# Performance work log

Hardware: AMD Instinct MI355X
Metric: run time of the kernel (lower is better)

## Reference

```python
import jax, jax.numpy as jnp
import numpy as np

N = 50000      # nodes
E = 600000     # edges
B = 64         # graphs in batch
DIN = 128      # input_dim
DH = 128       # hidden_dim
P = 32         # perm_length
C = 2          # num_classes
K = 2          # TAGConv hops (DGL default)


def setup_inputs() -> dict:
    key = jax.random.key(0)
    ks = jax.random.split(key, 12)
    h = jax.random.normal(ks[0], (N, DIN), dtype=jnp.float32)
    src = jax.random.randint(ks[1], (E,), 0, N, dtype=jnp.int64)
    dst = jax.random.randint(ks[2], (E,), 0, N, dtype=jnp.int64)
    graph_ids = jnp.sort(jax.random.randint(ks[3], (N,), 0, B, dtype=jnp.int64))
    perm_features = jax.random.normal(ks[4], (B, P), dtype=jnp.float32)
    s1 = 1.0 / np.sqrt((K + 1) * DIN)
    s2 = 1.0 / np.sqrt((K + 1) * DH)
    sc = 1.0 / np.sqrt(DH + P)
    W1 = jax.random.uniform(ks[5], ((K + 1) * DIN, DH), jnp.float32, -s1, s1)
    b1 = jax.random.uniform(ks[6], (DH,), jnp.float32, -s1, s1)
    W2 = jax.random.uniform(ks[7], ((K + 1) * DH, DH), jnp.float32, -s2, s2)
    b2 = jax.random.uniform(ks[8], (DH,), jnp.float32, -s2, s2)
    Wc = jax.random.uniform(ks[9], (DH + P, C), jnp.float32, -sc, sc)
    bc = jax.random.uniform(ks[10], (C,), jnp.float32, -sc, sc)
    return {"h": h, "src": src, "dst": dst, "graph_ids": graph_ids,
            "perm_features": perm_features, "W1": W1, "b1": b1,
            "W2": W2, "b2": b2, "Wc": Wc, "bc": bc}


def _tag_conv(x, src, dst, norm, W, b):
    feats = [x]
    for _ in range(K):
        m = jax.ops.segment_sum((feats[-1] * norm)[src], dst, num_segments=N)
        feats.append(m * norm)
    return jnp.concatenate(feats, axis=-1) @ W + b


def reference(h, src, dst, graph_ids, perm_features, W1, b1, W2, b2, Wc, bc):
    # symmetric norm from in-degrees, clamped at 1 (DGL convention)
    deg = jax.ops.segment_sum(jnp.ones((E,), h.dtype), dst, num_segments=N)
    norm = jnp.where(deg < 1.0, 1.0, deg)[:, None] ** -0.5  # [N,1]
    x = jax.nn.relu(_tag_conv(h, src, dst, norm, W1, b1))
    x = _tag_conv(x, src, dst, norm, W2, b2)
    # mean_nodes over batched graph
    sums = jax.ops.segment_sum(x, graph_ids, num_segments=B)          # [B,DH]
    cnt = jax.ops.segment_sum(jnp.ones((N,), x.dtype), graph_ids, num_segments=B)
    hg = sums / jnp.maximum(cnt, 1.0)[:, None]
    combined = jnp.concatenate([hg, perm_features], axis=1)           # [B,DH+P]
    return combined @ Wc + bc
```

## Files before the change

### kernel.cpp

```cpp
#include <hip/hip_runtime.h>

#define N_NODES 50000
#define N_EDGES 600000
#define B_GRAPHS 64
#define DH 128
#define PFEAT 32
#define NCLS 2
#define SCAN_BLOCKS ((N_NODES + 255) / 256)
#define NPAD (N_NODES + 128)

typedef __attribute__((ext_vector_type(8))) short short8v;
typedef __attribute__((ext_vector_type(4))) float float4v;
typedef __attribute__((ext_vector_type(4))) unsigned int uint4v;

__device__ __forceinline__ unsigned int f2bf(float f) {
    unsigned int u = __float_as_uint(f);
    return (u + 0x7FFFu + ((u >> 16) & 1u)) >> 16;
}
__device__ __forceinline__ float bflo(unsigned int p) { return __uint_as_float(p << 16); }
__device__ __forceinline__ float bfhi(unsigned int p) { return __uint_as_float(p & 0xFFFF0000u); }

__global__ void k_cvt(const float* __restrict__ in, unsigned short* __restrict__ outb, int n4) {
    int t = blockIdx.x * blockDim.x + threadIdx.x;
    if (t < n4) {
        float4 v = ((const float4*)in)[t];
        unsigned int lo = f2bf(v.x) | (f2bf(v.y) << 16);
        unsigned int hi = f2bf(v.z) | (f2bf(v.w) << 16);
        uint2 r; r.x = lo; r.y = hi;
        ((uint2*)outb)[t] = r;
    }
}

__global__ void k_cvt_w(const float* __restrict__ W, unsigned short* __restrict__ Wt) {
    int t = blockIdx.x * blockDim.x + threadIdx.x;
    if (t < 384 * 128) {
        int k = t >> 7, c = t & 127;
        Wt[c * 384 + k] = (unsigned short)f2bf(W[t]);
    }
}

__global__ void k_deg(const int* __restrict__ dst, int* __restrict__ deg) {
    int e = blockIdx.x * blockDim.x + threadIdx.x;
    if (e < N_EDGES) atomicAdd(&deg[dst[e]], 1);
}

__global__ void k_norm(const int* __restrict__ deg, float* __restrict__ norm) {
    int n = blockIdx.x * blockDim.x + threadIdx.x;
    if (n < N_NODES) {
        int d = deg[n];
        if (d < 1) d = 1;
        norm[n] = rsqrtf((float)d);
    }
}

__global__ void k_bound(const int* __restrict__ gid, int* __restrict__ gstart) {
    int n = blockIdx.x * blockDim.x + threadIdx.x;
    if (n < N_NODES) {
        int g = gid[n];
        if (n == 0 || gid[n - 1] != g) gstart[g] = n;
    }
}

__global__ void k_bsum(const int* __restrict__ deg, int* __restrict__ bsum) {
    __shared__ int s[256];
    int i = blockIdx.x * 256 + threadIdx.x;
    s[threadIdx.x] = (i < N_NODES) ? deg[i] : 0;
    __syncthreads();
    for (int off = 128; off > 0; off >>= 1) {
        if (threadIdx.x < off) s[threadIdx.x] += s[threadIdx.x + off];
        __syncthreads();
    }
    if (threadIdx.x == 0) bsum[blockIdx.x] = s[0];
}

__global__ void k_bscan(int* __restrict__ bsum) {
    __shared__ int s[256];
    int v = (threadIdx.x < SCAN_BLOCKS) ? bsum[threadIdx.x] : 0;
    s[threadIdx.x] = v;
    __syncthreads();
    for (int off = 1; off < 256; off <<= 1) {
        int t = (threadIdx.x >= off) ? s[threadIdx.x - off] : 0;
        __syncthreads();
        s[threadIdx.x] += t;
        __syncthreads();
    }
    if (threadIdx.x < SCAN_BLOCKS) bsum[threadIdx.x] = s[threadIdx.x] - v;
}

__global__ void k_scan2(const int* __restrict__ deg, const int* __restrict__ bsum,
                        int* __restrict__ row_ptr) {
    __shared__ int s[256];
    int i = blockIdx.x * 256 + threadIdx.x;
    int v = (i < N_NODES) ? deg[i] : 0;
    s[threadIdx.x] = v;
    __syncthreads();
    for (int off = 1; off < 256; off <<= 1) {
        int t = (threadIdx.x >= off) ? s[threadIdx.x - off] : 0;
        __syncthreads();
        s[threadIdx.x] += t;
        __syncthreads();
    }
    if (i < N_NODES) row_ptr[i + 1] = s[threadIdx.x] + bsum[blockIdx.x];
    if (i == 0) row_ptr[0] = 0;
}

__global__ void k_scatter(const int* __restrict__ src, const int* __restrict__ dst,
                          const int* __restrict__ row_ptr, int* __restrict__ cnt,
                          int* __restrict__ col) {
    int e = blockIdx.x * blockDim.x + threadIdx.x;
    if (e < N_EDGES) {
        int d = dst[e];
        int pos = atomicAdd(&cnt[d], 1);
        col[row_ptr[d] + pos] = src[e];
    }
}

__global__ __launch_bounds__(256) void k_spmm(const unsigned short* __restrict__ fin,
                                              const float* __restrict__ norm,
                                              const int* __restrict__ row_ptr,
                                              const int* __restrict__ col,
                                              unsigned short* __restrict__ fout) {
    int wave = threadIdx.x >> 6;
    int lane = threadIdx.x & 63;
    int grp = lane >> 4;
    int l15 = lane & 15;
    int v = blockIdx.x * 4 + wave;
    if (v >= N_NODES) return;
    int beg = row_ptr[v], end = row_ptr[v + 1];

    float a0[8], a1[8];
#pragma unroll
    for (int j = 0; j < 8; ++j) { a0[j] = 0.f; a1[j] = 0.f; }

    for (int base = beg; base < end; base += 8) {
        int e0 = base + grp;
        int e1 = base + 4 + grp;
        int ec0 = (e0 < end) ? e0 : end - 1;
        int ec1 = (e1 < end) ? e1 : end - 1;
        int u0 = col[ec0];
        int u1 = col[ec1];
        uint4v r0 = *(const uint4v*)(fin + (size_t)u0 * 128 + l15 * 8);
        uint4v r1 = *(const uint4v*)(fin + (size_t)u1 * 128 + l15 * 8);
        float w0 = (e0 < end) ? norm[u0] : 0.f;
        float w1 = (e1 < end) ? norm[u1] : 0.f;
#pragma unroll
        for (int q = 0; q < 4; ++q) {
            a0[2 * q]     = fmaf(bflo(r0[q]), w0, a0[2 * q]);
            a0[2 * q + 1] = fmaf(bfhi(r0[q]), w0, a0[2 * q + 1]);
            a1[2 * q]     = fmaf(bflo(r1[q]), w1, a1[2 * q]);
            a1[2 * q + 1] = fmaf(bfhi(r1[q]), w1, a1[2 * q + 1]);
        }
    }

#pragma unroll
    for (int j = 0; j < 8; ++j) {
        float s = a0[j] + a1[j];
        s += __shfl_xor(s, 16, 64);
        s += __shfl_xor(s, 32, 64);
        a0[j] = s;
    }
    if (grp == 0) {
        float nv = norm[v];
        uint4v o;
#pragma unroll
        for (int q = 0; q < 4; ++q)
            o[q] = f2bf(a0[2 * q] * nv) | (f2bf(a0[2 * q + 1] * nv) << 16);
        *(uint4v*)(fout + (size_t)v * 128 + l15 * 8) = o;
    }
}

template <bool RELU, bool POOL>
__global__ __launch_bounds__(256) void k_gemm_mfma(const unsigned short* __restrict__ A0,
                                                   const unsigned short* __restrict__ A1,
                                                   const unsigned short* __restrict__ A2,
                                                   const unsigned short* __restrict__ Wt,
                                                   const float* __restrict__ bias,
                                                   unsigned short* __restrict__ out,
                                                   const int* __restrict__ gid,
                                                   float* __restrict__ gsum) {
    __shared__ float red4[4][128];
    int tid = threadIdx.x;
    int lane = tid & 63;
    int wid = tid >> 6;
    int l15 = lane & 15;
    int lk = lane >> 4;
    int n0 = blockIdx.x * 128;
    int rbase = n0 + wid * 32;

    float4v acc[2][8];
#pragma unroll
    for (int rt = 0; rt < 2; ++rt)
#pragma unroll
        for (int ct = 0; ct < 8; ++ct)
#pragma unroll
            for (int i = 0; i < 4; ++i) acc[rt][ct][i] = 0.f;

    const unsigned short* Aseg[3] = {A0, A1, A2};
#pragma unroll
    for (int ks = 0; ks < 12; ++ks) {
        const unsigned short* A = Aseg[ks >> 2];
        int kloc = (ks & 3) * 32 + lk * 8;
        short8v a0 = *(const short8v*)(A + (size_t)(rbase + l15) * 128 + kloc);
        short8v a1 = *(const short8v*)(A + (size_t)(rbase + 16 + l15) * 128 + kloc);
        const unsigned short* wp = Wt + (size_t)l15 * 384 + ks * 32 + lk * 8;
#pragma unroll
        for (int ct = 0; ct < 8; ++ct) {
            short8v b = *(const short8v*)(wp + (size_t)ct * 16 * 384);
            acc[0][ct] = __builtin_amdgcn_mfma_f32_16x16x32_bf16(a0, b, acc[0][ct], 0, 0, 0);
            acc[1][ct] = __builtin_amdgcn_mfma_f32_16x16x32_bf16(a1, b, acc[1][ct], 0, 0, 0);
        }
    }

    if (!POOL) {
        float bj[8];
#pragma unroll
        for (int ct = 0; ct < 8; ++ct) bj[ct] = bias[ct * 16 + l15];
#pragma unroll
        for (int rt = 0; rt < 2; ++rt)
#pragma unroll
            for (int i = 0; i < 4; ++i) {
                int row = rbase + rt * 16 + lk * 4 + i;
                if (row < N_NODES) {
#pragma unroll
                    for (int ct = 0; ct < 8; ++ct) {
                        float v = acc[rt][ct][i] + bj[ct];
                        if (RELU) v = fmaxf(v, 0.f);
                        out[(size_t)row * 128 + ct * 16 + l15] = (unsigned short)f2bf(v);
                    }
                }
            }
    } else {
        int gr[2][4];
#pragma unroll
        for (int rt = 0; rt < 2; ++rt)
#pragma unroll
            for (int i = 0; i < 4; ++i) {
                int row = rbase + rt * 16 + lk * 4 + i;
                gr[rt][i] = (row < N_NODES) ? gid[row] : -1;
            }
        int lastrow = n0 + 127;
        if (lastrow >= N_NODES) lastrow = N_NODES - 1;
        int gfirst = gid[n0];
        int glast = gid[lastrow];
        for (int g = gfirst; g <= glast; ++g) {
            float p[8];
#pragma unroll
            for (int ct = 0; ct < 8; ++ct) {
                float s = 0.f;
#pragma unroll
                for (int rt = 0; rt < 2; ++rt)
#pragma unroll
                    for (int i = 0; i < 4; ++i)
                        if (gr[rt][i] == g) s += acc[rt][ct][i];
                p[ct] = s;
            }
#pragma unroll
            for (int ct = 0; ct < 8; ++ct) {
                p[ct] += __shfl_xor(p[ct], 16, 64);
                p[ct] += __shfl_xor(p[ct], 32, 64);
            }
            if (lane < 16) {
#pragma unroll
                for (int ct = 0; ct < 8; ++ct) red4[wid][ct * 16 + lane] = p[ct];
            }
            __syncthreads();
            if (tid < 128) {
                float s = red4[0][tid] + red4[1][tid] + red4[2][tid] + red4[3][tid];
                atomicAdd(&gsum[g * 128 + tid], s);
            }
            __syncthreads();
        }
    }
}

__global__ void k_final(const float* __restrict__ gsum, const int* __restrict__ gstart,
                        const float* __restrict__ b2, const float* __restrict__ perm,
                        const float* __restrict__ Wc, const float* __restrict__ bc,
                        float* __restrict__ out) {
    int t = threadIdx.x;
    if (t >= B_GRAPHS * NCLS) return;
    int b = t / NCLS, c = t % NCLS;
    int s = gstart[b];
    float cf = 1.f;
    bool nonempty = (s >= 0);
    if (nonempty) {
        int nxt = N_NODES;
        for (int j = b + 1; j < B_GRAPHS; ++j) {
            int sj = gstart[j];
            if (sj >= 0) { nxt = sj; break; }
        }
        int cnt = nxt - s;
        cf = (cnt < 1) ? 1.f : (float)cnt;
    }
    float acc = bc[c];
    for (int d = 0; d < DH; ++d) {
        float hg = gsum[b * 128 + d] / cf + (nonempty ? b2[d] : 0.f);
        acc += hg * Wc[d * NCLS + c];
    }
    for (int p = 0; p < PFEAT; ++p) acc += perm[b * PFEAT + p] * Wc[(DH + p) * NCLS + c];
    out[t] = acc;
}

extern "C" void kernel_launch(void* const* d_in, const int* in_sizes, int n_in,
                              void* d_out, int out_size, void* d_ws, size_t ws_size,
                              hipStream_t stream) {
    const float* h    = (const float*)d_in[0];
    const int*   src  = (const int*)d_in[1];
    const int*   dst  = (const int*)d_in[2];
    const int*   gid  = (const int*)d_in[3];
    const float* perm = (const float*)d_in[4];
    const float* W1   = (const float*)d_in[5];
    const float* b1   = (const float*)d_in[6];
    const float* W2   = (const float*)d_in[7];
    const float* b2   = (const float*)d_in[8];
    const float* Wc   = (const float*)d_in[9];
    const float* bc   = (const float*)d_in[10];
    float* out = (float*)d_out;

    char* ws = (char*)d_ws;
    size_t off = 0;
    auto alloc = [&](size_t bytes) {
        void* p = ws + off;
        off = (off + bytes + 255) & ~(size_t)255;
        return p;
    };
    int*   deg     = (int*)alloc(N_NODES * 4);
    int*   cnt     = (int*)alloc(N_NODES * 4);
    int*   row_ptr = (int*)alloc((N_NODES + 1) * 4);
    int*   col     = (int*)alloc(N_EDGES * 4);
    int*   bsum    = (int*)alloc(SCAN_BLOCKS * 4);
    float* norm    = (float*)alloc(N_NODES * 4);
    unsigned short* h_bf = (unsigned short*)alloc((size_t)NPAD * 128 * 2);
    unsigned short* f1   = (unsigned short*)alloc((size_t)NPAD * 128 * 2);
    unsigned short* f2   = (unsigned short*)alloc((size_t)NPAD * 128 * 2);
    unsigned short* x2   = (unsigned short*)alloc((size_t)NPAD * 128 * 2);
    unsigned short* Wt1  = (unsigned short*)alloc(384 * 128 * 2);
    unsigned short* Wt2  = (unsigned short*)alloc(384 * 128 * 2);
    float* gsum    = (float*)alloc(B_GRAPHS * 128 * 4);
    int*   gstart  = (int*)alloc(B_GRAPHS * 4);

    hipMemsetAsync(deg, 0, N_NODES * 4, stream);
    hipMemsetAsync(cnt, 0, N_NODES * 4, stream);
    hipMemsetAsync(gsum, 0, B_GRAPHS * 128 * 4, stream);
    hipMemsetAsync(gstart, 0xFF, B_GRAPHS * 4, stream);

    k_cvt<<<(N_NODES * 128 / 4 + 255) / 256, 256, 0, stream>>>(h, h_bf, N_NODES * 128 / 4);
    k_cvt_w<<<(384 * 128 + 255) / 256, 256, 0, stream>>>(W1, Wt1);
    k_cvt_w<<<(384 * 128 + 255) / 256, 256, 0, stream>>>(W2, Wt2);

    k_deg<<<(N_EDGES + 255) / 256, 256, 0, stream>>>(dst, deg);
    k_norm<<<(N_NODES + 255) / 256, 256, 0, stream>>>(deg, norm);
    k_bound<<<(N_NODES + 255) / 256, 256, 0, stream>>>(gid, gstart);
    k_bsum<<<SCAN_BLOCKS, 256, 0, stream>>>(deg, bsum);
    k_bscan<<<1, 256, 0, stream>>>(bsum);
    k_scan2<<<SCAN_BLOCKS, 256, 0, stream>>>(deg, bsum, row_ptr);
    k_scatter<<<(N_EDGES + 255) / 256, 256, 0, stream>>>(src, dst, row_ptr, cnt, col);

    int spmm_grid = (N_NODES + 3) / 4;
    int gemm_grid = (N_NODES + 127) / 128;

    k_spmm<<<spmm_grid, 256, 0, stream>>>(h_bf, norm, row_ptr, col, f1);
    k_spmm<<<spmm_grid, 256, 0, stream>>>(f1, norm, row_ptr, col, f2);
    k_gemm_mfma<true, false><<<gemm_grid, 256, 0, stream>>>(h_bf, f1, f2, Wt1, b1, x2, gid, gsum);

    k_spmm<<<spmm_grid, 256, 0, stream>>>(x2, norm, row_ptr, col, f1);
    k_spmm<<<spmm_grid, 256, 0, stream>>>(f1, norm, row_ptr, col, f2);
    k_gemm_mfma<false, true><<<gemm_grid, 256, 0, stream>>>(x2, f1, f2, Wt2, nullptr, nullptr, gid, gsum);

    k_final<<<1, 128, 0, stream>>>(gsum, gstart, b2, perm, Wc, bc, out);
}
```

Before: 278.5 us.

## Fuse preprocessing kernels and memsets; unroll SpMM edge loop to four accumulators

Merges the four memsets, the input and weight bf16 conversions, the degree count and graph-boundary detection, and the norm computation with the block sum into three kernels, cutting about eight launches from the preprocessing chain. The SpMM inner loop now handles 16 edges per iteration with four independent accumulator sets, so more gather loads are in flight per wave. The cost is more registers in the SpMM kernel and more wasted clamped loads for low-degree nodes, since the average degree is about 12.

```diff
diff --git a/kernel.cpp b/kernel.cpp
--- a/kernel.cpp
+++ b/kernel.cpp
@@ -8,6 +8,8 @@
 #define NCLS 2
 #define SCAN_BLOCKS ((N_NODES + 255) / 256)
 #define NPAD (N_NODES + 128)
+#define NCVT4 (N_NODES * 128 / 4)
+#define WELEMS (384 * 128)
 
 typedef __attribute__((ext_vector_type(8))) short short8v;
 typedef __attribute__((ext_vector_type(4))) float float4v;
@@ -20,51 +22,50 @@
 __device__ __forceinline__ float bflo(unsigned int p) { return __uint_as_float(p << 16); }
 __device__ __forceinline__ float bfhi(unsigned int p) { return __uint_as_float(p & 0xFFFF0000u); }
 
-__global__ void k_cvt(const float* __restrict__ in, unsigned short* __restrict__ outb, int n4) {
-    int t = blockIdx.x * blockDim.x + threadIdx.x;
-    if (t < n4) {
-        float4 v = ((const float4*)in)[t];
+__global__ void k_init(const float* __restrict__ h, unsigned short* __restrict__ h_bf,
+                       const float* __restrict__ W1, const float* __restrict__ W2,
+                       unsigned short* __restrict__ Wt1, unsigned short* __restrict__ Wt2,
+                       int* __restrict__ deg, int* __restrict__ cnt,
+                       float* __restrict__ gsum, int* __restrict__ gstart) {
+    int t = blockIdx.x * 256 + threadIdx.x;
+    if (t < NCVT4) {
+        float4 v = ((const float4*)h)[t];
         unsigned int lo = f2bf(v.x) | (f2bf(v.y) << 16);
         unsigned int hi = f2bf(v.z) | (f2bf(v.w) << 16);
         uint2 r; r.x = lo; r.y = hi;
-        ((uint2*)outb)[t] = r;
-    }
-}
-
-__global__ void k_cvt_w(const float* __restrict__ W, unsigned short* __restrict__ Wt) {
-    int t = blockIdx.x * blockDim.x + threadIdx.x;
-    if (t < 384 * 128) {
-        int k = t >> 7, c = t & 127;
-        Wt[c * 384 + k] = (unsigned short)f2bf(W[t]);
-    }
-}
-
-__global__ void k_deg(const int* __restrict__ dst, int* __restrict__ deg) {
-    int e = blockIdx.x * blockDim.x + threadIdx.x;
-    if (e < N_EDGES) atomicAdd(&deg[dst[e]], 1);
-}
-
-__global__ void k_norm(const int* __restrict__ deg, float* __restrict__ norm) {
-    int n = blockIdx.x * blockDim.x + threadIdx.x;
-    if (n < N_NODES) {
-        int d = deg[n];
-        if (d < 1) d = 1;
-        norm[n] = rsqrtf((float)d);
-    }
-}
-
-__global__ void k_bound(const int* __restrict__ gid, int* __restrict__ gstart) {
-    int n = blockIdx.x * blockDim.x + threadIdx.x;
-    if (n < N_NODES) {
+        ((uint2*)h_bf)[t] = r;
+    }
+    if (t < 2 * WELEMS) {
+        bool second = (t >= WELEMS);
+        int idx = second ? t - WELEMS : t;
+        const float* W = second ? W2 : W1;
+        unsigned short* Wt = second ? Wt2 : Wt1;
+        int k = idx >> 7, c = idx & 127;
+        Wt[c * 384 + k] = (unsigned short)f2bf(W[idx]);
+    }
+    if (t < N_NODES) { deg[t] = 0; cnt[t] = 0; }
+    if (t < B_GRAPHS * DH) gsum[t] = 0.f;
+    if (t < B_GRAPHS) gstart[t] = -1;
+}
+
+__global__ void k_deg_bound(const int* __restrict__ dst, const int* __restrict__ gid,
+                            int* __restrict__ deg, int* __restrict__ gstart) {
+    int t = blockIdx.x * 256 + threadIdx.x;
+    if (t < N_EDGES) atomicAdd(&deg[dst[t]], 1);
+    int n = t - N_EDGES;
+    if (n >= 0 && n < N_NODES) {
         int g = gid[n];
         if (n == 0 || gid[n - 1] != g) gstart[g] = n;
     }
 }
 
-__global__ void k_bsum(const int* __restrict__ deg, int* __restrict__ bsum) {
+__global__ void k_norm_bsum(const int* __restrict__ deg, float* __restrict__ norm,
+                            int* __restrict__ bsum) {
     __shared__ int s[256];
     int i = blockIdx.x * 256 + threadIdx.x;
-    s[threadIdx.x] = (i < N_NODES) ? deg[i] : 0;
+    int d = (i < N_NODES) ? deg[i] : 0;
+    if (i < N_NODES) norm[i] = rsqrtf((float)(d < 1 ? 1 : d));
+    s[threadIdx.x] = d;
     __syncthreads();
     for (int off = 128; off > 0; off >>= 1) {
         if (threadIdx.x < off) s[threadIdx.x] += s[threadIdx.x + off];
@@ -128,33 +129,43 @@
     if (v >= N_NODES) return;
     int beg = row_ptr[v], end = row_ptr[v + 1];
 
-    float a0[8], a1[8];
-#pragma unroll
-    for (int j = 0; j < 8; ++j) { a0[j] = 0.f; a1[j] = 0.f; }
-
-    for (int base = beg; base < end; base += 8) {
+    float a0[8], a1[8], a2[8], a3[8];
+#pragma unroll
+    for (int j = 0; j < 8; ++j) { a0[j] = 0.f; a1[j] = 0.f; a2[j] = 0.f; a3[j] = 0.f; }
+
+    for (int base = beg; base < end; base += 16) {
         int e0 = base + grp;
-        int e1 = base + 4 + grp;
-        int ec0 = (e0 < end) ? e0 : end - 1;
-        int ec1 = (e1 < end) ? e1 : end - 1;
-        int u0 = col[ec0];
-        int u1 = col[ec1];
+        int e1 = e0 + 4, e2 = e0 + 8, e3 = e0 + 12;
+        int last = end - 1;
+        int c0 = (e0 < end) ? e0 : last;
+        int c1 = (e1 < end) ? e1 : last;
+        int c2 = (e2 < end) ? e2 : last;
+        int c3 = (e3 < end) ? e3 : last;
+        int u0 = col[c0], u1 = col[c1], u2 = col[c2], u3 = col[c3];
         uint4v r0 = *(const uint4v*)(fin + (size_t)u0 * 128 + l15 * 8);
         uint4v r1 = *(const uint4v*)(fin + (size_t)u1 * 128 + l15 * 8);
+        uint4v r2 = *(const uint4v*)(fin + (size_t)u2 * 128 + l15 * 8);
+        uint4v r3 = *(const uint4v*)(fin + (size_t)u3 * 128 + l15 * 8);
         float w0 = (e0 < end) ? norm[u0] : 0.f;
         float w1 = (e1 < end) ? norm[u1] : 0.f;
+        float w2 = (e2 < end) ? norm[u2] : 0.f;
+        float w3 = (e3 < end) ? norm[u3] : 0.f;
 #pragma unroll
         for (int q = 0; q < 4; ++q) {
             a0[2 * q]     = fmaf(bflo(r0[q]), w0, a0[2 * q]);
             a0[2 * q + 1] = fmaf(bfhi(r0[q]), w0, a0[2 * q + 1]);
             a1[2 * q]     = fmaf(bflo(r1[q]), w1, a1[2 * q]);
             a1[2 * q + 1] = fmaf(bfhi(r1[q]), w1, a1[2 * q + 1]);
+            a2[2 * q]     = fmaf(bflo(r2[q]), w2, a2[2 * q]);
+            a2[2 * q + 1] = fmaf(bfhi(r2[q]), w2, a2[2 * q + 1]);
+            a3[2 * q]     = fmaf(bflo(r3[q]), w3, a3[2 * q]);
+            a3[2 * q + 1] = fmaf(bfhi(r3[q]), w3, a3[2 * q + 1]);
         }
     }
 
 #pragma unroll
     for (int j = 0; j < 8; ++j) {
-        float s = a0[j] + a1[j];
+        float s = (a0[j] + a1[j]) + (a2[j] + a3[j]);
         s += __shfl_xor(s, 16, 64);
         s += __shfl_xor(s, 32, 64);
         a0[j] = s;
@@ -339,19 +350,10 @@
     float* gsum    = (float*)alloc(B_GRAPHS * 128 * 4);
     int*   gstart  = (int*)alloc(B_GRAPHS * 4);
 
-    hipMemsetAsync(deg, 0, N_NODES * 4, stream);
-    hipMemsetAsync(cnt, 0, N_NODES * 4, stream);
-    hipMemsetAsync(gsum, 0, B_GRAPHS * 128 * 4, stream);
-    hipMemsetAsync(gstart, 0xFF, B_GRAPHS * 4, stream);
-
-    k_cvt<<<(N_NODES * 128 / 4 + 255) / 256, 256, 0, stream>>>(h, h_bf, N_NODES * 128 / 4);
-    k_cvt_w<<<(384 * 128 + 255) / 256, 256, 0, stream>>>(W1, Wt1);
-    k_cvt_w<<<(384 * 128 + 255) / 256, 256, 0, stream>>>(W2, Wt2);
-
-    k_deg<<<(N_EDGES + 255) / 256, 256, 0, stream>>>(dst, deg);
-    k_norm<<<(N_NODES + 255) / 256, 256, 0, stream>>>(deg, norm);
-    k_bound<<<(N_NODES + 255) / 256, 256, 0, stream>>>(gid, gstart);
-    k_bsum<<<SCAN_BLOCKS, 256, 0, stream>>>(deg, bsum);
+    k_init<<<(NCVT4 + 255) / 256, 256, 0, stream>>>(h, h_bf, W1, W2, Wt1, Wt2,
+                                                    deg, cnt, gsum, gstart);
+    k_deg_bound<<<(N_EDGES + N_NODES + 255) / 256, 256, 0, stream>>>(dst, gid, deg, gstart);
+    k_norm_bsum<<<SCAN_BLOCKS, 256, 0, stream>>>(deg, norm, bsum);
     k_bscan<<<1, 256, 0, stream>>>(bsum);
     k_scan2<<<SCAN_BLOCKS, 256, 0, stream>>>(deg, bsum, row_ptr);
     k_scatter<<<(N_EDGES + 255) / 256, 256, 0, stream>>>(src, dst, row_ptr, cnt, col);
```

New measurement: 269.9 us. -3.1%, faster.
